# Kernel tuning notes

Measured on AMD Instinct MI355X. Metric: run time of the kernel, lower is better.

Reference implementation:

```python
import jax, jax.numpy as jnp
import numpy as np

KH, KW = 7, 7            # extraction kernel
EH, EW = 5, 5            # effective (cropped) kernel
PAD = (KH - EH) // 2     # = 1
EPS = 1e-7


def _extract_patches(x):
    # x: [B,H,W,C] -> patches [B,Ho,Wo,KH,KW,C], stride 1, VALID padding
    B, H, Wd, C = x.shape
    Ho, Wo = H - KH + 1, Wd - KW + 1
    rows = []
    for i in range(KH):
        cols = [x[:, i:i + Ho, j:j + Wo, :] for j in range(KW)]
        rows.append(jnp.stack(cols, axis=3))          # [B,Ho,Wo,KW,C]
    return jnp.stack(rows, axis=3)                     # [B,Ho,Wo,KH,KW,C]


def _rotate_bilinear(patches, angles):
    # patches: [N,KH,KW,C]; angles: [N]. Mirrors tf.contrib.image
    # angles_to_projective_transforms + transform(BILINEAR, fill=0).
    # Note: the layer's det(matrix)==0 NEAREST fallback never fires (det==1).
    N = patches.shape[0]
    c, s = jnp.cos(angles), jnp.sin(angles)
    Wm1, Hm1 = jnp.float32(KW - 1), jnp.float32(KH - 1)
    xo = (Wm1 - (c * Wm1 - s * Hm1)) * 0.5
    yo = (Hm1 - (s * Wm1 + c * Hm1)) * 0.5
    scale = jnp.float32(1.0 + EPS)   # transforms /= transforms[:,8:9]+1e-7
    a0, a1, a2 = c / scale, -s / scale, xo / scale
    a3, a4, a5 = s / scale, c / scale, yo / scale
    yg, xg = jnp.meshgrid(jnp.arange(KH, dtype=jnp.float32),
                          jnp.arange(KW, dtype=jnp.float32), indexing='ij')
    x_in = a0[:, None, None] * xg + a1[:, None, None] * yg + a2[:, None, None]
    y_in = a3[:, None, None] * xg + a4[:, None, None] * yg + a5[:, None, None]
    x0f = jnp.floor(x_in); y0f = jnp.floor(y_in)
    wx1 = x_in - x0f; wx0 = 1.0 - wx1
    wy1 = y_in - y0f; wy0 = 1.0 - wy1
    x0 = x0f.astype(jnp.int32); x1 = x0 + 1
    y0 = y0f.astype(jnp.int32); y1 = y0 + 1
    nidx = jnp.arange(N)[:, None, None]

    def corner(yi, xi, w):
        valid = ((xi >= 0) & (xi < KW) & (yi >= 0) & (yi < KH)).astype(patches.dtype)
        v = patches[nidx, jnp.clip(yi, 0, KH - 1), jnp.clip(xi, 0, KW - 1)]
        return (w * valid)[..., None] * v

    return (corner(y0, x0, wy0 * wx0) + corner(y0, x1, wy0 * wx1) +
            corner(y1, x0, wy1 * wx0) + corner(y1, x1, wy1 * wx1))


def reference(x, W, b):
    B, H, Wd, C = x.shape
    patches = _extract_patches(x)                      # [B,Ho,Wo,KH,KW,C]
    _, Ho, Wo = patches.shape[:3]
    intensity = jnp.sum(patches, axis=-1)              # [B,Ho,Wo,KH,KW]
    row_idx = jnp.repeat(jnp.arange(KH, dtype=jnp.float32), KW)   # rowMulti
    col_idx = jnp.tile(jnp.arange(KW, dtype=jnp.float32), KH)     # colMulti
    flat = intensity.reshape(-1, KH * KW)              # [N, KH*KW]
    denom = jnp.sum(flat, -1) + EPS
    cr = jnp.sum(flat * row_idx, -1) / denom - (KH - 1) / 2.0
    cc = jnp.sum(flat * col_idx, -1) / denom - (KW - 1) / 2.0
    angle = jnp.arctan2(cr, cc + EPS)                  # [N]
    patches_n = patches.reshape(-1, KH, KW, C)         # [N,KH,KW,C]
    rot = _rotate_bilinear(patches_n, angle)
    rot = rot[:, PAD:PAD + EH, PAD:PAD + EW, :]        # crop to effective
    rot = rot.reshape(B, Ho, Wo, EH * EW * C)
    w_flat = W.reshape(W.shape[0], -1)                 # [F, EH*EW*C]
    out = jnp.einsum('bhwk,fk->bhwf', rot, w_flat) + b
    return out


def setup_inputs() -> dict:
    key = jax.random.key(0)
    kx, kw, _ = jax.random.split(key, 3)
    x = jax.random.normal(kx, (8, 64, 64, 32), dtype=jnp.float32)
    W = jax.random.normal(kw, (64, EH, EW, 32), dtype=jnp.float32) * 0.05
    b = jnp.zeros((64,), dtype=jnp.float32)
    return {"x": x, "W": W, "b": b}
```

## Files before the change

### kernel.cpp

```cpp
#include <hip/hip_runtime.h>
#include <hip/hip_bf16.h>

#define EPSF 1e-7f
#define B_ 8
#define H_ 64
#define W_ 64
#define C_ 32
#define HO 58
#define WO 58
#define NF 64
#define KDIM 800

#define XBS 40
#define RS  808

typedef __bf16 v8bf __attribute__((ext_vector_type(8)));
typedef float  v4f  __attribute__((ext_vector_type(4)));

__global__ void k_wpack(const float* __restrict__ W, __bf16* __restrict__ Wp) {
    int t = blockIdx.x*256 + threadIdx.x;
    int j = t & 7; int lane = (t >> 3) & 63; int rest = t >> 9;
    int kb = rest % 25; int nt = rest / 25;
    int f = nt*16 + (lane & 15);
    int k = kb*32 + (lane >> 4)*8 + j;
    Wp[t] = (__bf16)W[f*KDIM + k];
}

__global__ __launch_bounds__(256, 4)
void k_main(const float* __restrict__ x, const v8bf* __restrict__ Wp,
            const float* __restrict__ bias, float* __restrict__ out) {
    __shared__ __bf16 xtb[7][22][XBS];
    __shared__ __bf16 rot[16][RS];
    __shared__ float  Srow[7][22];
    __shared__ float4 pp[16];

    int tid = threadIdx.x;
    int wv = tid >> 6, lane = tid & 63;
    int m = lane & 15, q = lane >> 4;

    {
    }
    int L = blockIdx.x + 4*(blockIdx.y + 58*blockIdx.z);
    int newL = (L & 7)*232 + (L >> 3);
    int b  = newL / 232;
    int rem = newL - b*232;
    int ho = rem >> 2;
    int wt = rem & 3;

    int wo0 = wt*16;
    int npx = WO - wo0; if (npx > 16) npx = 16;
    int ncols = npx + 6;

    float bv = bias[wv*16 + m];

    if (tid < 7*ncols) {
        int r, c;
        if (ncols == 22) { r = tid/22; c = tid - r*22; }
        else             { r = tid >> 4; c = tid & 15; }
        const float* src = x + (size_t)((b*H_ + ho + r)*W_ + wo0 + c)*C_;
        float4 vq[8];
#pragma unroll
        for (int qq = 0; qq < 8; qq++) vq[qq] = *(const float4*)(src + qq*4);
        float s = 0.f;
#pragma unroll
        for (int qq = 0; qq < 8; qq++) s += vq[qq].x + vq[qq].y + vq[qq].z + vq[qq].w;
        Srow[r][c] = s;
#pragma unroll
        for (int h8 = 0; h8 < 4; h8++) {
            v8bf o;
            o[0]=(__bf16)vq[h8*2].x;   o[1]=(__bf16)vq[h8*2].y;
            o[2]=(__bf16)vq[h8*2].z;   o[3]=(__bf16)vq[h8*2].w;
            o[4]=(__bf16)vq[h8*2+1].x; o[5]=(__bf16)vq[h8*2+1].y;
            o[6]=(__bf16)vq[h8*2+1].z; o[7]=(__bf16)vq[h8*2+1].w;
            *(v8bf*)&xtb[r][c][h8*8] = o;
        }
    }
    __syncthreads();

    if (tid < npx) {
        float den = 0.f, crn = 0.f, ccn = 0.f;
#pragma unroll
        for (int i = 0; i < 7; i++)
#pragma unroll
            for (int j = 0; j < 7; j++) {
                float v = Srow[i][tid + j];
                den += v; crn += v*(float)i; ccn += v*(float)j;
            }
        float dt = den + EPSF;
        float cr = crn/dt - 3.0f;
        float cx = ccn/dt - 3.0f + EPSF;
        float r2 = cr*cr + cx*cx;
        float inv = r2 > 0.f ? rsqrtf(r2) : 0.f;
        float c = r2 > 0.f ? cx*inv : 1.0f;
        float s = cr*inv;
        const float scale = 1.0f + EPSF;
        float xo = (6.0f - (c*6.0f - s*6.0f))*0.5f;
        float yo = (6.0f - (s*6.0f + c*6.0f))*0.5f;
        pp[tid] = make_float4(c/scale, s/scale, xo/scale, yo/scale);
    }
    __syncthreads();

    for (int e = tid; e < 400; e += 256) {
        int px = e & 15; int pos = e >> 4;
        if (px < npx) {
            int py = pos/5; int yy = py + 1; int xx = pos - py*5 + 1;
            float4 p = pp[px];
            float xin = p.x*(float)xx - p.y*(float)yy + p.z;
            float yin = p.y*(float)xx + p.x*(float)yy + p.w;
            float x0f = floorf(xin), y0f = floorf(yin);
            float wx1 = xin - x0f, wx0 = 1.0f - wx1;
            float wy1 = yin - y0f, wy0 = 1.0f - wy1;
            int ix0 = (int)x0f, iy0 = (int)y0f;
            int ix1 = ix0 + 1,  iy1 = iy0 + 1;

            const __bf16* bp[4]; float wgt[4];
            auto mkcorner = [&](int yi, int xi, float w, int idx) {
                bool valid = (xi >= 0) & (xi < 7) & (yi >= 0) & (yi < 7);
                int cy = yi < 0 ? 0 : (yi > 6 ? 6 : yi);
                int cx2 = xi < 0 ? 0 : (xi > 6 ? 6 : xi);
                bp[idx]  = &xtb[cy][px + cx2][0];
                wgt[idx] = valid ? w : 0.0f;
            };
            mkcorner(iy0, ix0, wy0*wx0, 0);
            mkcorner(iy0, ix1, wy0*wx1, 1);
            mkcorner(iy1, ix0, wy1*wx0, 2);
            mkcorner(iy1, ix1, wy1*wx1, 3);

            float accx[16], accy[16];
#pragma unroll
            for (int i = 0; i < 16; i++) { accx[i] = 0.f; accy[i] = 0.f; }
#pragma unroll
            for (int cn = 0; cn < 4; cn++) {
                const __bf16* src = bp[cn]; float wq = wgt[cn];
#pragma unroll
                for (int q8 = 0; q8 < 4; q8++) {
                    union { v8bf v; unsigned u[4]; } uv;
                    uv.v = *(const v8bf*)(src + q8*8);
#pragma unroll
                    for (int j = 0; j < 4; j++) {
                        float lo = __uint_as_float(uv.u[j] << 16);
                        float hi = __uint_as_float(uv.u[j] & 0xffff0000u);
                        accx[q8*4+j] += wq*lo;
                        accy[q8*4+j] += wq*hi;
                    }
                }
            }
#pragma unroll
            for (int q8 = 0; q8 < 4; q8++) {
                v8bf o;
#pragma unroll
                for (int j = 0; j < 4; j++) {
                    o[2*j]   = (__bf16)accx[q8*4+j];
                    o[2*j+1] = (__bf16)accy[q8*4+j];
                }
                *(v8bf*)&rot[px][pos*32 + q8*8] = o;
            }
        }
    }

    const v8bf* wp = Wp + (size_t)wv*25*64 + lane;
    v8bf bfA[13];
#pragma unroll
    for (int kb = 0; kb < 13; kb++) bfA[kb] = wp[kb*64];
    __syncthreads();

    v8bf bfB[12];
#pragma unroll
    for (int kb = 0; kb < 12; kb++) bfB[kb] = wp[(13 + kb)*64];

    v4f acc0 = {0.f, 0.f, 0.f, 0.f};
    v4f acc1 = {0.f, 0.f, 0.f, 0.f};
#pragma unroll
    for (int kb = 0; kb < 12; kb++) {
        v8bf a0 = *(const v8bf*)&rot[m][kb*32 + q*8];
        acc0 = __builtin_amdgcn_mfma_f32_16x16x32_bf16(a0, bfA[kb], acc0, 0, 0, 0);
        v8bf a1 = *(const v8bf*)&rot[m][(13 + kb)*32 + q*8];
        acc1 = __builtin_amdgcn_mfma_f32_16x16x32_bf16(a1, bfB[kb], acc1, 0, 0, 0);
    }
    {
        v8bf a0 = *(const v8bf*)&rot[m][12*32 + q*8];
        acc0 = __builtin_amdgcn_mfma_f32_16x16x32_bf16(a0, bfA[12], acc0, 0, 0, 0);
    }

    int f = wv*16 + m;
    int pixbase = (b*HO + ho)*WO + wo0;
#pragma unroll
    for (int r = 0; r < 4; r++) {
        int px = q*4 + r;
        if (px < npx) out[(size_t)(pixbase + px)*NF + f] = acc0[r] + acc1[r] + bv;
    }
}

extern "C" void kernel_launch(void* const* d_in, const int* in_sizes, int n_in,
                              void* d_out, int out_size, void* d_ws, size_t ws_size,
                              hipStream_t stream) {
    const float* x    = (const float*)d_in[0];
    const float* W    = (const float*)d_in[1];
    const float* bias = (const float*)d_in[2];
    float* out = (float*)d_out;
    __bf16* Wp = (__bf16*)d_ws;

    k_wpack<<<dim3(200), 256, 0, stream>>>(W, Wp);
    k_main<<<dim3(4, HO, B_), 256, 0, stream>>>(x, (const v8bf*)Wp, bias, out);
}
```

Baseline: 78.30 us.

## Parallelize centroid reduction across lanes and fuse angle into rotation stage

```diff
diff --git a/kernel.cpp b/kernel.cpp
--- a/kernel.cpp
+++ b/kernel.cpp
@@ -16,6 +16,7 @@
 
 typedef __bf16 v8bf __attribute__((ext_vector_type(8)));
 typedef float  v4f  __attribute__((ext_vector_type(4)));
+typedef float  v2f  __attribute__((ext_vector_type(2)));
 
 __global__ void k_wpack(const float* __restrict__ W, __bf16* __restrict__ Wp) {
     int t = blockIdx.x*256 + threadIdx.x;
@@ -32,14 +33,11 @@
     __shared__ __bf16 xtb[7][22][XBS];
     __shared__ __bf16 rot[16][RS];
     __shared__ float  Srow[7][22];
-    __shared__ float4 pp[16];
 
     int tid = threadIdx.x;
     int wv = tid >> 6, lane = tid & 63;
     int m = lane & 15, q = lane >> 4;
 
-    {
-    }
     int L = blockIdx.x + 4*(blockIdx.y + 58*blockIdx.z);
     int newL = (L & 7)*232 + (L >> 3);
     int b  = newL / 232;
@@ -77,15 +75,25 @@
     }
     __syncthreads();
 
-    if (tid < npx) {
-        float den = 0.f, crn = 0.f, ccn = 0.f;
-#pragma unroll
-        for (int i = 0; i < 7; i++)
-#pragma unroll
-            for (int j = 0; j < 7; j++) {
-                float v = Srow[i][tid + j];
-                den += v; crn += v*(float)i; ccn += v*(float)j;
-            }
+    int pxl = wv*4 + q;
+    float den = 0.f, crn = 0.f, ccn = 0.f;
+#pragma unroll
+    for (int k = 0; k < 4; k++) {
+        int t = m + 16*k;
+        if (t < 49) {
+            int i = t / 7, j = t - 7*i;
+            float v = Srow[i][pxl + j];
+            den += v; crn += v*(float)i; ccn += v*(float)j;
+        }
+    }
+#pragma unroll
+    for (int msk = 1; msk <= 8; msk <<= 1) {
+        den += __shfl_xor(den, msk);
+        crn += __shfl_xor(crn, msk);
+        ccn += __shfl_xor(ccn, msk);
+    }
+    float pc, ps, pxo, pyo;
+    {
         float dt = den + EPSF;
         float cr = crn/dt - 3.0f;
         float cx = ccn/dt - 3.0f + EPSF;
@@ -94,19 +102,18 @@
         float c = r2 > 0.f ? cx*inv : 1.0f;
         float s = cr*inv;
         const float scale = 1.0f + EPSF;
-        float xo = (6.0f - (c*6.0f - s*6.0f))*0.5f;
-        float yo = (6.0f - (s*6.0f + c*6.0f))*0.5f;
-        pp[tid] = make_float4(c/scale, s/scale, xo/scale, yo/scale);
-    }
-    __syncthreads();
-
-    for (int e = tid; e < 400; e += 256) {
-        int px = e & 15; int pos = e >> 4;
-        if (px < npx) {
+        pc  = c/scale; ps = s/scale;
+        pxo = (6.0f - (c*6.0f - s*6.0f))*0.5f/scale;
+        pyo = (6.0f - (s*6.0f + c*6.0f))*0.5f/scale;
+    }
+
+#pragma unroll
+    for (int rnd = 0; rnd < 2; rnd++) {
+        int pos = m + 16*rnd;
+        if (pos < 25) {
             int py = pos/5; int yy = py + 1; int xx = pos - py*5 + 1;
-            float4 p = pp[px];
-            float xin = p.x*(float)xx - p.y*(float)yy + p.z;
-            float yin = p.y*(float)xx + p.x*(float)yy + p.w;
+            float xin = pc*(float)xx - ps*(float)yy + pxo;
+            float yin = ps*(float)xx + pc*(float)yy + pyo;
             float x0f = floorf(xin), y0f = floorf(yin);
             float wx1 = xin - x0f, wx0 = 1.0f - wx1;
             float wy1 = yin - y0f, wy0 = 1.0f - wy1;
@@ -118,7 +125,7 @@
                 bool valid = (xi >= 0) & (xi < 7) & (yi >= 0) & (yi < 7);
                 int cy = yi < 0 ? 0 : (yi > 6 ? 6 : yi);
                 int cx2 = xi < 0 ? 0 : (xi > 6 ? 6 : xi);
-                bp[idx]  = &xtb[cy][px + cx2][0];
+                bp[idx]  = &xtb[cy][pxl + cx2][0];
                 wgt[idx] = valid ? w : 0.0f;
             };
             mkcorner(iy0, ix0, wy0*wx0, 0);
@@ -126,22 +133,22 @@
             mkcorner(iy1, ix0, wy1*wx0, 2);
             mkcorner(iy1, ix1, wy1*wx1, 3);
 
-            float accx[16], accy[16];
-#pragma unroll
-            for (int i = 0; i < 16; i++) { accx[i] = 0.f; accy[i] = 0.f; }
+            v2f acc[16];
+#pragma unroll
+            for (int i = 0; i < 16; i++) acc[i] = (v2f){0.f, 0.f};
 #pragma unroll
             for (int cn = 0; cn < 4; cn++) {
-                const __bf16* src = bp[cn]; float wq = wgt[cn];
+                const __bf16* src = bp[cn];
+                v2f wq2 = (v2f){wgt[cn], wgt[cn]};
 #pragma unroll
                 for (int q8 = 0; q8 < 4; q8++) {
                     union { v8bf v; unsigned u[4]; } uv;
                     uv.v = *(const v8bf*)(src + q8*8);
 #pragma unroll
-                    for (int j = 0; j < 4; j++) {
-                        float lo = __uint_as_float(uv.u[j] << 16);
-                        float hi = __uint_as_float(uv.u[j] & 0xffff0000u);
-                        accx[q8*4+j] += wq*lo;
-                        accy[q8*4+j] += wq*hi;
+                    for (int d = 0; d < 4; d++) {
+                        v2f val = (v2f){ __uint_as_float(uv.u[d] << 16),
+                                         __uint_as_float(uv.u[d] & 0xffff0000u) };
+                        acc[q8*4 + d] += wq2 * val;
                     }
                 }
             }
@@ -149,11 +156,11 @@
             for (int q8 = 0; q8 < 4; q8++) {
                 v8bf o;
 #pragma unroll
-                for (int j = 0; j < 4; j++) {
-                    o[2*j]   = (__bf16)accx[q8*4+j];
-                    o[2*j+1] = (__bf16)accy[q8*4+j];
+                for (int d = 0; d < 4; d++) {
+                    o[2*d]   = (__bf16)acc[q8*4 + d].x;
+                    o[2*d+1] = (__bf16)acc[q8*4 + d].y;
                 }
-                *(v8bf*)&rot[px][pos*32 + q8*8] = o;
+                *(v8bf*)&rot[pxl][pos*32 + q8*8] = o;
             }
         }
     }
```

Result: faster. 76.17 us (-2.7%).
